# Optimization experiments

Hardware: AMD Instinct MI355X
Metric: run time of the kernel (lower is better)

The kernel has to match this reference:

```python
import jax, jax.numpy as jnp
import numpy as np

DIN = 256
HID = 512

def setup_inputs() -> dict:
    key = jax.random.key(0)
    ks = jax.random.split(key, 9)
    s_in = 1.0 / np.sqrt(DIN)
    s_h = 1.0 / np.sqrt(HID)
    h = jax.random.normal(ks[0], (32, 1024, DIN), dtype=jnp.float32)
    Wv = jax.random.uniform(ks[1], (HID, DIN), jnp.float32, -s_in, s_in)
    bv = jax.random.uniform(ks[2], (HID,), jnp.float32, -s_in, s_in)
    Wk = jax.random.uniform(ks[3], (HID, DIN), jnp.float32, -s_in, s_in)
    bk = jax.random.uniform(ks[4], (HID,), jnp.float32, -s_in, s_in)
    Wq = jax.random.uniform(ks[5], (HID, DIN), jnp.float32, -s_in, s_in)
    bq = jax.random.uniform(ks[6], (HID,), jnp.float32, -s_in, s_in)
    Wo = jax.random.uniform(ks[7], (DIN, HID), jnp.float32, -s_h, s_h)
    bo = jax.random.uniform(ks[8], (DIN,), jnp.float32, -s_h, s_h)
    return {"h": h, "Wv": Wv, "bv": bv, "Wk": Wk, "bk": bk, "Wq": Wq, "bq": bq, "Wo": Wo, "bo": bo}

def reference(h, Wv, bv, Wk, bk, Wq, bq, Wo, bo):
    # relu-activated Q/K/V projections: [B, N, HID]
    v = jax.nn.relu(jnp.einsum('bnd,hd->bnh', h, Wv) + bv)
    q = jax.nn.relu(jnp.einsum('bnd,hd->bnh', h, Wq) + bq)
    k = jax.nn.relu(jnp.einsum('bnd,hd->bnh', h, Wk) + bk)
    # unscaled attention: [B, N, N]
    att = jax.nn.softmax(jnp.einsum('bnh,bmh->bnm', q, k), axis=2)
    out = jnp.einsum('bnm,bmh->bnh', att, v)          # [B, N, HID]
    out = jax.nn.relu(jnp.einsum('bnh,dh->bnd', out, Wo) + bo)  # [B, N, DIN]
    return out
```

## Files before the change

### kernel.cpp

```cpp
#include <hip/hip_runtime.h>
#include <cstdint>
#include <cstddef>

#define NB    32
#define SEQ   1024
#define DIN   256
#define HID   512
#define MTOT  32768
#define KQLD  1024

typedef _Float16 half_t;
typedef _Float16 half8  __attribute__((ext_vector_type(8)));
typedef _Float16 half4v __attribute__((ext_vector_type(4)));
typedef float    f32x4  __attribute__((ext_vector_type(4)));

typedef __attribute__((address_space(1))) const void* gas_ptr;
typedef __attribute__((address_space(3))) void*       las_ptr;

__global__ void cvt_all(const float* __restrict__ h,
                        const float* __restrict__ Wv, const float* __restrict__ Wk,
                        const float* __restrict__ Wq, const float* __restrict__ Wo,
                        const float* __restrict__ bv, const float* __restrict__ bk,
                        const float* __restrict__ bq,
                        half_t* __restrict__ h16, half_t* __restrict__ W16,
                        half_t* __restrict__ Wo16, float* __restrict__ biasq) {
    int b = blockIdx.x;
    if (b < 8192) {
        int i = b * 256 + threadIdx.x;
        f32x4 v = ((const f32x4*)h)[i];
        half4v o;
        o[0] = (half_t)v[0]; o[1] = (half_t)v[1]; o[2] = (half_t)v[2]; o[3] = (half_t)v[3];
        ((half4v*)h16)[i] = o;
    } else if (b < 8704) {
        int w = (b - 8192) >> 7;
        int i = ((b - 8192) & 127) * 256 + threadIdx.x;
        const float* s = w == 0 ? Wv : w == 1 ? Wk : w == 2 ? Wq : Wo;
        half_t*      d = w < 3 ? W16 + (size_t)w * HID * DIN : Wo16;
        f32x4 v = ((const f32x4*)s)[i];
        half4v o;
        o[0] = (half_t)v[0]; o[1] = (half_t)v[1]; o[2] = (half_t)v[2]; o[3] = (half_t)v[3];
        ((half4v*)d)[i] = o;
    } else {
        for (int i = threadIdx.x; i < HID; i += 256) {
            biasq[i]           = bv[i];
            biasq[HID + i]     = bk[i];
            biasq[2 * HID + i] = bq[i];
        }
    }
}

__global__ __launch_bounds__(256, 2) void kq_k(
    const half_t* __restrict__ A, const half_t* __restrict__ Bw,
    const float* __restrict__ biasq, half_t* __restrict__ kq16)
{
    __shared__ alignas(16) half_t As[128 * 32];
    __shared__ alignas(16) half_t Bs[256 * 32];

    const int t    = threadIdx.x;
    const int lane = t & 63;
    const int wave = t >> 6;
    const int wm   = wave >> 1;
    const int wn   = wave & 1;
    const int lanen = lane & 15;
    const int quad  = lane >> 4;
    const long m0 = (long)blockIdx.x * 128;
    const long n0 = (long)blockIdx.y * 256;

    const half_t* gA[2]; half_t* lA[2];
    const half_t* gB[4]; half_t* lB[4];
#pragma unroll
    for (int s = 0; s < 2; s++) {
        int c = t + 256 * s;
        gA[s] = A + (m0 + (c >> 2)) * DIN + (c & 3) * 8;
        lA[s] = &As[c * 8];
    }
#pragma unroll
    for (int s = 0; s < 4; s++) {
        int c = t + 256 * s;
        gB[s] = Bw + (n0 + (c >> 2)) * DIN + (c & 3) * 8;
        lB[s] = &Bs[c * 8];
    }

    int aoff[4], boff[8];
#pragma unroll
    for (int i = 0; i < 4; i++) aoff[i] = (wm * 64 + i * 16 + lanen) * 32 + quad * 8;
#pragma unroll
    for (int j = 0; j < 8; j++) boff[j] = (wn * 128 + j * 16 + lanen) * 32 + quad * 8;

    f32x4 acc[4][8];
#pragma unroll
    for (int i = 0; i < 4; i++)
#pragma unroll
        for (int j = 0; j < 8; j++)
            acc[i][j] = f32x4{0.f, 0.f, 0.f, 0.f};

    for (int k0 = 0; k0 < DIN; k0 += 32) {
#pragma unroll
        for (int s = 0; s < 2; s++)
            __builtin_amdgcn_global_load_lds((gas_ptr)(gA[s] + k0), (las_ptr)lA[s], 16, 0, 0);
#pragma unroll
        for (int s = 0; s < 4; s++)
            __builtin_amdgcn_global_load_lds((gas_ptr)(gB[s] + k0), (las_ptr)lB[s], 16, 0, 0);
        __syncthreads();
        half8 af[4], bf[8];
#pragma unroll
        for (int i = 0; i < 4; i++) af[i] = *(const half8*)&As[aoff[i]];
#pragma unroll
        for (int j = 0; j < 8; j++) bf[j] = *(const half8*)&Bs[boff[j]];
#pragma unroll
        for (int i = 0; i < 4; i++)
#pragma unroll
            for (int j = 0; j < 8; j++)
                acc[i][j] = __builtin_amdgcn_mfma_f32_16x16x32_f16(bf[j], af[i], acc[i][j], 0, 0, 0);
        __syncthreads();
    }

#pragma unroll
    for (int i = 0; i < 4; i++) {
        long mrow = m0 + wm * 64 + i * 16 + lanen;
#pragma unroll
        for (int j = 0; j < 8; j++) {
            long gn = n0 + wn * 128 + j * 16 + quad * 4;
            f32x4 bb = *(const f32x4*)&biasq[HID + gn];
            f32x4 v = acc[i][j];
            half4v pk;
#pragma unroll
            for (int r = 0; r < 4; r++) pk[r] = (half_t)fmaxf(v[r] + bb[r], 0.f);
            *(half4v*)(kq16 + mrow * KQLD + gn) = pk;
        }
    }
}

__global__ __launch_bounds__(256, 2) void v_k(
    const half_t* __restrict__ A, const half_t* __restrict__ Bw,
    const float* __restrict__ biasq, half_t* __restrict__ vT)
{
    __shared__ alignas(16) half_t As[128 * 32];
    __shared__ alignas(16) half_t Bs[256 * 32];

    const int t    = threadIdx.x;
    const int lane = t & 63;
    const int wave = t >> 6;
    const int wm   = wave >> 1;
    const int wn   = wave & 1;
    const int lanen = lane & 15;
    const int quad  = lane >> 4;
    const long m0 = (long)blockIdx.x * 128;
    const long n0 = (long)blockIdx.y * 256;

    const half_t* gA[2]; half_t* lA[2];
    const half_t* gB[4]; half_t* lB[4];
#pragma unroll
    for (int s = 0; s < 2; s++) {
        int c = t + 256 * s;
        gA[s] = A + (m0 + (c >> 2)) * DIN + (c & 3) * 8;
        lA[s] = &As[c * 8];
    }
#pragma unroll
    for (int s = 0; s < 4; s++) {
        int c = t + 256 * s;
        gB[s] = Bw + (n0 + (c >> 2)) * DIN + (c & 3) * 8;
        lB[s] = &Bs[c * 8];
    }

    int aoff[4], boff[8];
#pragma unroll
    for (int i = 0; i < 4; i++) aoff[i] = (wm * 64 + i * 16 + lanen) * 32 + quad * 8;
#pragma unroll
    for (int j = 0; j < 8; j++) boff[j] = (wn * 128 + j * 16 + lanen) * 32 + quad * 8;

    f32x4 acc[4][8];
#pragma unroll
    for (int i = 0; i < 4; i++)
#pragma unroll
        for (int j = 0; j < 8; j++)
            acc[i][j] = f32x4{0.f, 0.f, 0.f, 0.f};

    for (int k0 = 0; k0 < DIN; k0 += 32) {
#pragma unroll
        for (int s = 0; s < 2; s++)
            __builtin_amdgcn_global_load_lds((gas_ptr)(gA[s] + k0), (las_ptr)lA[s], 16, 0, 0);
#pragma unroll
        for (int s = 0; s < 4; s++)
            __builtin_amdgcn_global_load_lds((gas_ptr)(gB[s] + k0), (las_ptr)lB[s], 16, 0, 0);
        __syncthreads();
        half8 af[4], bf[8];
#pragma unroll
        for (int i = 0; i < 4; i++) af[i] = *(const half8*)&As[aoff[i]];
#pragma unroll
        for (int j = 0; j < 8; j++) bf[j] = *(const half8*)&Bs[boff[j]];
#pragma unroll
        for (int i = 0; i < 4; i++)
#pragma unroll
            for (int j = 0; j < 8; j++)
                acc[i][j] = __builtin_amdgcn_mfma_f32_16x16x32_f16(af[i], bf[j], acc[i][j], 0, 0, 0);
        __syncthreads();
    }

#pragma unroll
    for (int i = 0; i < 4; i++) {
        long mrow = m0 + wm * 64 + i * 16 + quad * 4;
        long bidx = mrow >> 10;
        long pos  = mrow & 1023;
#pragma unroll
        for (int j = 0; j < 8; j++) {
            long gn = n0 + wn * 128 + j * 16 + lanen;
            float bb = biasq[gn];
            f32x4 v = acc[i][j];
            half4v pk;
#pragma unroll
            for (int r = 0; r < 4; r++) pk[r] = (half_t)fmaxf(v[r] + bb, 0.f);
            *(half4v*)(vT + ((bidx * HID + gn) << 10) + pos) = pk;
        }
    }
}

__global__ __launch_bounds__(256, 2) void se_k(
    const half_t* __restrict__ KQ,
    half_t* __restrict__ E, float* __restrict__ Mstat, float* __restrict__ Lstat)
{
    __shared__ alignas(16) half_t As[128 * 32];
    __shared__ alignas(16) half_t Bs[256 * 32];

    const int t    = threadIdx.x;
    const int lane = t & 63;
    const int wave = t >> 6;
    const int wm   = wave >> 1;
    const int wn   = wave & 1;
    const int lanen = lane & 15;
    const int quad  = lane >> 4;
    const int z     = blockIdx.z;
    const long m0 = (long)blockIdx.x * 128;
    const long n0 = (long)blockIdx.y * 256;

    const half_t* Ab = KQ + (long)z * SEQ * KQLD + HID;
    const half_t* Bb = KQ + (long)z * SEQ * KQLD;

    f32x4 acc[4][8];
#pragma unroll
    for (int i = 0; i < 4; i++)
#pragma unroll
        for (int j = 0; j < 8; j++)
            acc[i][j] = f32x4{0.f, 0.f, 0.f, 0.f};

    const half_t* gA[2]; half_t* lA[2];
    const half_t* gB[4]; half_t* lB[4];
#pragma unroll
    for (int s = 0; s < 2; s++) {
        int c = t + 256 * s;
        gA[s] = Ab + (m0 + (c >> 2)) * KQLD + (c & 3) * 8;
        lA[s] = &As[c * 8];
    }
#pragma unroll
    for (int s = 0; s < 4; s++) {
        int c = t + 256 * s;
        gB[s] = Bb + (n0 + (c >> 2)) * KQLD + (c & 3) * 8;
        lB[s] = &Bs[c * 8];
    }

    int aoff[4], boff[8];
#pragma unroll
    for (int i = 0; i < 4; i++) aoff[i] = (wm * 64 + i * 16 + lanen) * 32 + quad * 8;
#pragma unroll
    for (int j = 0; j < 8; j++) boff[j] = (wn * 128 + j * 16 + lanen) * 32 + quad * 8;

    for (int k0 = 0; k0 < HID; k0 += 32) {
#pragma unroll
        for (int s = 0; s < 2; s++)
            __builtin_amdgcn_global_load_lds((gas_ptr)(gA[s] + k0), (las_ptr)lA[s], 16, 0, 0);
#pragma unroll
        for (int s = 0; s < 4; s++)
            __builtin_amdgcn_global_load_lds((gas_ptr)(gB[s] + k0), (las_ptr)lB[s], 16, 0, 0);
        __syncthreads();

        half8 af[4], bf[8];
#pragma unroll
        for (int i = 0; i < 4; i++) af[i] = *(const half8*)&As[aoff[i]];
#pragma unroll
        for (int j = 0; j < 8; j++) bf[j] = *(const half8*)&Bs[boff[j]];
#pragma unroll
        for (int i = 0; i < 4; i++)
#pragma unroll
            for (int j = 0; j < 8; j++)
                acc[i][j] = __builtin_amdgcn_mfma_f32_16x16x32_f16(bf[j], af[i], acc[i][j], 0, 0, 0);
        __syncthreads();
    }

    float mf[4];
#pragma unroll
    for (int i = 0; i < 4; i++) {
        float v = acc[i][0][0];
#pragma unroll
        for (int j = 0; j < 8; j++)
#pragma unroll
            for (int r = 0; r < 4; r++) v = fmaxf(v, acc[i][j][r]);
        v = fmaxf(v, __shfl_xor(v, 16, 64));
        v = fmaxf(v, __shfl_xor(v, 32, 64));
        mf[i] = v;
    }

    half_t* Eb = E + (long)z * SEQ * SEQ;
    float rs[4] = {0.f, 0.f, 0.f, 0.f};
#pragma unroll
    for (int i = 0; i < 4; i++) {
        long qrow = m0 + wm * 64 + i * 16 + lanen;
#pragma unroll
        for (int j = 0; j < 8; j++) {
            long gn = n0 + wn * 128 + j * 16 + quad * 4;
            half4v hv;
#pragma unroll
            for (int r = 0; r < 4; r++) {
                float e = __expf(acc[i][j][r] - mf[i]);
                rs[i] += e;
                hv[r] = (half_t)e;
            }
            *(half4v*)(Eb + qrow * SEQ + gn) = hv;
        }
    }
#pragma unroll
    for (int i = 0; i < 4; i++) {
        float v = rs[i];
        v += __shfl_xor(v, 16, 64);
        v += __shfl_xor(v, 32, 64);
        rs[i] = v;
    }

    if (quad == 0) {
        long base = ((long)z * 8 + blockIdx.y * 2 + wn) * SEQ + m0 + wm * 64;
#pragma unroll
        for (int i = 0; i < 4; i++) {
            Mstat[base + i * 16 + lanen] = mf[i];
            Lstat[base + i * 16 + lanen] = rs[i];
        }
    }
}

__global__ __launch_bounds__(256, 2) void pv_k(
    const half_t* __restrict__ E, const half_t* __restrict__ vT,
    const float* __restrict__ Mstat, const float* __restrict__ Lstat,
    half_t* __restrict__ O16)
{
    __shared__ alignas(16) half_t As[128 * 32];
    __shared__ alignas(16) half_t Bs[256 * 32];
    __shared__ float scaleS[8][128];
    __shared__ float invS[128];

    const int t    = threadIdx.x;
    const int lane = t & 63;
    const int wave = t >> 6;
    const int wm   = wave >> 1;
    const int wn   = wave & 1;
    const int lanen = lane & 15;
    const int quad  = lane >> 4;
    const int z     = blockIdx.z;
    const long m0 = (long)blockIdx.x * 128;
    const long h0 = (long)blockIdx.y * 256;

    if (t < 128) {
        float mv[8];
        float M = -1e30f;
#pragma unroll
        for (int kb = 0; kb < 8; kb++) {
            mv[kb] = Mstat[((long)z * 8 + kb) * SEQ + m0 + t];
            M = fmaxf(M, mv[kb]);
        }
        float ls = 0.f;
#pragma unroll
        for (int kb = 0; kb < 8; kb++) {
            float sc = __expf(mv[kb] - M);
            scaleS[kb][t] = sc;
            ls += Lstat[((long)z * 8 + kb) * SEQ + m0 + t] * sc;
        }
        invS[t] = 1.f / ls;
    }
    __syncthreads();

    const half_t* Ab = E  + (long)z * SEQ * SEQ;
    const half_t* Bb = vT + (long)z * HID * SEQ;

    f32x4 acc[4][8];
#pragma unroll
    for (int i = 0; i < 4; i++)
#pragma unroll
        for (int j = 0; j < 8; j++)
            acc[i][j] = f32x4{0.f, 0.f, 0.f, 0.f};

    const half_t* gA[2]; half_t* lA[2];
    const half_t* gB[4]; half_t* lB[4];
#pragma unroll
    for (int s = 0; s < 2; s++) {
        int c = t + 256 * s;
        gA[s] = Ab + (m0 + (c >> 2)) * SEQ + (c & 3) * 8;
        lA[s] = &As[c * 8];
    }
#pragma unroll
    for (int s = 0; s < 4; s++) {
        int c = t + 256 * s;
        gB[s] = Bb + (h0 + (c >> 2)) * SEQ + (c & 3) * 8;
        lB[s] = &Bs[c * 8];
    }

    int aoff[4], boff[8];
#pragma unroll
    for (int i = 0; i < 4; i++) aoff[i] = (wm * 64 + i * 16 + lanen) * 32 + quad * 8;
#pragma unroll
    for (int j = 0; j < 8; j++) boff[j] = (wn * 128 + j * 16 + lanen) * 32 + quad * 8;

    for (int k0 = 0; k0 < SEQ; k0 += 32) {
#pragma unroll
        for (int s = 0; s < 2; s++)
            __builtin_amdgcn_global_load_lds((gas_ptr)(gA[s] + k0), (las_ptr)lA[s], 16, 0, 0);
#pragma unroll
        for (int s = 0; s < 4; s++)
            __builtin_amdgcn_global_load_lds((gas_ptr)(gB[s] + k0), (las_ptr)lB[s], 16, 0, 0);
        __syncthreads();

        const int kb = k0 >> 7;
        half8 af[4], bf[8];
#pragma unroll
        for (int i = 0; i < 4; i++) {
            af[i] = *(const half8*)&As[aoff[i]];
            half_t sh = (half_t)scaleS[kb][wm * 64 + i * 16 + lanen];
            af[i] *= sh;
        }
#pragma unroll
        for (int j = 0; j < 8; j++) bf[j] = *(const half8*)&Bs[boff[j]];
#pragma unroll
        for (int i = 0; i < 4; i++)
#pragma unroll
            for (int j = 0; j < 8; j++)
                acc[i][j] = __builtin_amdgcn_mfma_f32_16x16x32_f16(bf[j], af[i], acc[i][j], 0, 0, 0);
        __syncthreads();
    }

    half_t* o = O16 + (long)z * SEQ * KQLD;
#pragma unroll
    for (int i = 0; i < 4; i++) {
        int qrl = wm * 64 + i * 16 + lanen;
        long qrow = m0 + qrl;
        float inv = invS[qrl];
#pragma unroll
        for (int j = 0; j < 8; j++) {
            long gn = h0 + wn * 128 + j * 16 + quad * 4;
            half4v hv;
#pragma unroll
            for (int r = 0; r < 4; r++) hv[r] = (half_t)(acc[i][j][r] * inv);
            *(half4v*)(o + qrow * KQLD + gn) = hv;
        }
    }
}

__global__ __launch_bounds__(256, 2) void oproj_k(
    const half_t* __restrict__ A, const half_t* __restrict__ Bw,
    float* __restrict__ Out, const float* __restrict__ bias)
{
    __shared__ alignas(16) half_t As[128 * 32];
    __shared__ alignas(16) half_t Bs[128 * 32];

    const int t    = threadIdx.x;
    const int lane = t & 63;
    const int wave = t >> 6;
    const int wm   = wave >> 1;
    const int wn   = wave & 1;
    const int lanen = lane & 15;
    const int quad  = lane >> 4;
    const long m0 = (long)blockIdx.x * 128;
    const long n0 = (long)blockIdx.y * 128;

    f32x4 acc[4][4];
#pragma unroll
    for (int i = 0; i < 4; i++)
#pragma unroll
        for (int j = 0; j < 4; j++)
            acc[i][j] = f32x4{0.f, 0.f, 0.f, 0.f};

    const int c0 = t, c1 = t + 256;
    const half_t* gA0 = A  + (m0 + (c0 >> 2)) * KQLD + (c0 & 3) * 8;
    const half_t* gA1 = A  + (m0 + (c1 >> 2)) * KQLD + (c1 & 3) * 8;
    const half_t* gB0 = Bw + (n0 + (c0 >> 2)) * HID + (c0 & 3) * 8;
    const half_t* gB1 = Bw + (n0 + (c1 >> 2)) * HID + (c1 & 3) * 8;
    half_t* lA0 = &As[c0 * 8];
    half_t* lA1 = &As[c1 * 8];
    half_t* lB0 = &Bs[c0 * 8];
    half_t* lB1 = &Bs[c1 * 8];

    int aoff[4], boff[4];
#pragma unroll
    for (int i = 0; i < 4; i++) aoff[i] = (wm * 64 + i * 16 + lanen) * 32 + quad * 8;
#pragma unroll
    for (int j = 0; j < 4; j++) boff[j] = (wn * 64 + j * 16 + lanen) * 32 + quad * 8;

    for (int k0 = 0; k0 < HID; k0 += 32) {
        __builtin_amdgcn_global_load_lds((gas_ptr)(gA0 + k0), (las_ptr)lA0, 16, 0, 0);
        __builtin_amdgcn_global_load_lds((gas_ptr)(gA1 + k0), (las_ptr)lA1, 16, 0, 0);
        __builtin_amdgcn_global_load_lds((gas_ptr)(gB0 + k0), (las_ptr)lB0, 16, 0, 0);
        __builtin_amdgcn_global_load_lds((gas_ptr)(gB1 + k0), (las_ptr)lB1, 16, 0, 0);
        __syncthreads();

        half8 af[4], bf[4];
#pragma unroll
        for (int i = 0; i < 4; i++) af[i] = *(const half8*)&As[aoff[i]];
#pragma unroll
        for (int j = 0; j < 4; j++) bf[j] = *(const half8*)&Bs[boff[j]];
#pragma unroll
        for (int i = 0; i < 4; i++)
#pragma unroll
            for (int j = 0; j < 4; j++)
                acc[i][j] = __builtin_amdgcn_mfma_f32_16x16x32_f16(bf[j], af[i], acc[i][j], 0, 0, 0);
        __syncthreads();
    }

#pragma unroll
    for (int i = 0; i < 4; i++) {
        long mrow = m0 + wm * 64 + i * 16 + lanen;
#pragma unroll
        for (int j = 0; j < 4; j++) {
            long gn = n0 + wn * 64 + j * 16 + quad * 4;
            f32x4 bb = *(const f32x4*)&bias[gn];
            f32x4 v = acc[i][j];
            f32x4 ov;
#pragma unroll
            for (int r = 0; r < 4; r++) ov[r] = fmaxf(v[r] + bb[r], 0.f);
            *(f32x4*)&Out[mrow * DIN + gn] = ov;
        }
    }
}

extern "C" void kernel_launch(void* const* d_in, const int* in_sizes, int n_in,
                              void* d_out, int out_size, void* d_ws, size_t ws_size,
                              hipStream_t stream) {
    const float* h  = (const float*)d_in[0];
    const float* Wv = (const float*)d_in[1];
    const float* bv = (const float*)d_in[2];
    const float* Wk = (const float*)d_in[3];
    const float* bk = (const float*)d_in[4];
    const float* Wq = (const float*)d_in[5];
    const float* bq = (const float*)d_in[6];
    const float* Wo = (const float*)d_in[7];
    const float* bo = (const float*)d_in[8];

    uint8_t* ws = (uint8_t*)d_ws;
    size_t off = 0;
    auto alloc = [&](size_t bytes) { size_t o = off; off += (bytes + 255) & ~(size_t)255; return o; };

    half_t* W16   = (half_t*)(ws + alloc((size_t)3 * HID * DIN * 2));
    half_t* Wo16  = (half_t*)(ws + alloc((size_t)DIN * HID * 2));
    float*  biasq = (float*)(ws + alloc((size_t)3 * HID * 4));
    half_t* kq16  = (half_t*)(ws + alloc((size_t)MTOT * KQLD * 2));
    half_t* vT    = (half_t*)(ws + alloc((size_t)MTOT * HID * 2));
    size_t h16_off = alloc((size_t)MTOT * DIN * 2);
    half_t* h16   = (half_t*)(ws + h16_off);
    half_t* O16 = kq16;

    size_t s_avail = ws_size > h16_off ? ws_size - h16_off : 0;
    size_t per_batch = (size_t)SEQ * SEQ * 2 + 2 * 8 * SEQ * 4;
    int GB = (int)(s_avail / per_batch);
    if (GB > NB) GB = NB;
    if (GB < 1)  GB = 1;
    half_t* Ebuf  = (half_t*)(ws + h16_off);
    float*  Mstat = (float*)(ws + h16_off + (size_t)GB * SEQ * SEQ * 2);
    float*  Lstat = Mstat + (size_t)GB * 8 * SEQ;

    cvt_all<<<dim3(8705), 256, 0, stream>>>(h, Wv, Wk, Wq, Wo, bv, bk, bq,
                                            h16, W16, Wo16, biasq);

    kq_k<<<dim3(MTOT / 128, 4), 256, 0, stream>>>(h16, W16 + (size_t)HID * DIN, biasq, kq16);
    v_k<<<dim3(MTOT / 128, 2), 256, 0, stream>>>(h16, W16, biasq, vT);

    for (int g0 = 0; g0 < NB; g0 += GB) {
        int gb = NB - g0 < GB ? NB - g0 : GB;
        se_k<<<dim3(SEQ / 128, SEQ / 256, gb), 256, 0, stream>>>(
            kq16 + (size_t)g0 * SEQ * KQLD,
            Ebuf, Mstat, Lstat);
        pv_k<<<dim3(SEQ / 128, HID / 256, gb), 256, 0, stream>>>(
            Ebuf, vT + (size_t)g0 * HID * SEQ,
            Mstat, Lstat,
            O16 + (size_t)g0 * SEQ * KQLD);
    }

    oproj_k<<<dim3(MTOT / 128, DIN / 128), 256, 0, stream>>>(O16, Wo16, (float*)d_out, bo);

    (void)in_sizes; (void)n_in; (void)out_size;
}
```

Before: 310.3 us.

## Double-buffer LDS tiles to overlap global-to-LDS loads with MFMA in all GEMMs

Every GEMM kernel (K/Q projection, V projection, score/exp, PV, output projection) now uses two LDS buffers for its A and B tiles. The first tile is loaded before the loop, and each iteration prefetches the next k-slice into the other buffer right after the barrier. The trailing per-iteration barrier is removed, and so is the separate barrier after the scale setup in the PV kernel. The aim is to hide global_load_lds latency behind MFMA work and halve the number of barriers. In exchange, LDS use per block doubles, which could limit occupancy.

Measured after the change: 315.1 us. Within noise of the previous version (+1.6%).

```diff
diff --git a/kernel.cpp b/kernel.cpp
--- a/kernel.cpp
+++ b/kernel.cpp
@@ -53,8 +53,8 @@
     const half_t* __restrict__ A, const half_t* __restrict__ Bw,
     const float* __restrict__ biasq, half_t* __restrict__ kq16)
 {
-    __shared__ alignas(16) half_t As[128 * 32];
-    __shared__ alignas(16) half_t Bs[256 * 32];
+    __shared__ alignas(16) half_t As[2][128 * 32];
+    __shared__ alignas(16) half_t Bs[2][256 * 32];
 
     const int t    = threadIdx.x;
     const int lane = t & 63;
@@ -66,19 +66,19 @@
     const long m0 = (long)blockIdx.x * 128;
     const long n0 = (long)blockIdx.y * 256;
 
-    const half_t* gA[2]; half_t* lA[2];
-    const half_t* gB[4]; half_t* lB[4];
+    const half_t* gA[2]; const half_t* gB[4];
+    int lAo[2], lBo[4];
 #pragma unroll
     for (int s = 0; s < 2; s++) {
         int c = t + 256 * s;
         gA[s] = A + (m0 + (c >> 2)) * DIN + (c & 3) * 8;
-        lA[s] = &As[c * 8];
+        lAo[s] = c * 8;
     }
 #pragma unroll
     for (int s = 0; s < 4; s++) {
         int c = t + 256 * s;
         gB[s] = Bw + (n0 + (c >> 2)) * DIN + (c & 3) * 8;
-        lB[s] = &Bs[c * 8];
+        lBo[s] = c * 8;
     }
 
     int aoff[4], boff[8];
@@ -94,25 +94,36 @@
         for (int j = 0; j < 8; j++)
             acc[i][j] = f32x4{0.f, 0.f, 0.f, 0.f};
 
-    for (int k0 = 0; k0 < DIN; k0 += 32) {
-#pragma unroll
-        for (int s = 0; s < 2; s++)
-            __builtin_amdgcn_global_load_lds((gas_ptr)(gA[s] + k0), (las_ptr)lA[s], 16, 0, 0);
-#pragma unroll
-        for (int s = 0; s < 4; s++)
-            __builtin_amdgcn_global_load_lds((gas_ptr)(gB[s] + k0), (las_ptr)lB[s], 16, 0, 0);
+#pragma unroll
+    for (int s = 0; s < 2; s++)
+        __builtin_amdgcn_global_load_lds((gas_ptr)gA[s], (las_ptr)&As[0][lAo[s]], 16, 0, 0);
+#pragma unroll
+    for (int s = 0; s < 4; s++)
+        __builtin_amdgcn_global_load_lds((gas_ptr)gB[s], (las_ptr)&Bs[0][lBo[s]], 16, 0, 0);
+
+#pragma unroll 2
+    for (int it = 0; it < DIN / 32; ++it) {
+        const int cur = it & 1;
         __syncthreads();
+        if (it + 1 < DIN / 32) {
+            const int k1 = (it + 1) * 32;
+#pragma unroll
+            for (int s = 0; s < 2; s++)
+                __builtin_amdgcn_global_load_lds((gas_ptr)(gA[s] + k1), (las_ptr)&As[cur ^ 1][lAo[s]], 16, 0, 0);
+#pragma unroll
+            for (int s = 0; s < 4; s++)
+                __builtin_amdgcn_global_load_lds((gas_ptr)(gB[s] + k1), (las_ptr)&Bs[cur ^ 1][lBo[s]], 16, 0, 0);
+        }
         half8 af[4], bf[8];
 #pragma unroll
-        for (int i = 0; i < 4; i++) af[i] = *(const half8*)&As[aoff[i]];
-#pragma unroll
-        for (int j = 0; j < 8; j++) bf[j] = *(const half8*)&Bs[boff[j]];
+        for (int i = 0; i < 4; i++) af[i] = *(const half8*)&As[cur][aoff[i]];
+#pragma unroll
+        for (int j = 0; j < 8; j++) bf[j] = *(const half8*)&Bs[cur][boff[j]];
 #pragma unroll
         for (int i = 0; i < 4; i++)
 #pragma unroll
             for (int j = 0; j < 8; j++)
                 acc[i][j] = __builtin_amdgcn_mfma_f32_16x16x32_f16(bf[j], af[i], acc[i][j], 0, 0, 0);
-        __syncthreads();
     }
 
 #pragma unroll
@@ -135,8 +146,8 @@
     const half_t* __restrict__ A, const half_t* __restrict__ Bw,
     const float* __restrict__ biasq, half_t* __restrict__ vT)
 {
-    __shared__ alignas(16) half_t As[128 * 32];
-    __shared__ alignas(16) half_t Bs[256 * 32];
+    __shared__ alignas(16) half_t As[2][128 * 32];
+    __shared__ alignas(16) half_t Bs[2][256 * 32];
 
     const int t    = threadIdx.x;
     const int lane = t & 63;
@@ -148,19 +159,19 @@
     const long m0 = (long)blockIdx.x * 128;
     const long n0 = (long)blockIdx.y * 256;
 
-    const half_t* gA[2]; half_t* lA[2];
-    const half_t* gB[4]; half_t* lB[4];
+    const half_t* gA[2]; const half_t* gB[4];
+    int lAo[2], lBo[4];
 #pragma unroll
     for (int s = 0; s < 2; s++) {
         int c = t + 256 * s;
         gA[s] = A + (m0 + (c >> 2)) * DIN + (c & 3) * 8;
-        lA[s] = &As[c * 8];
+        lAo[s] = c * 8;
     }
 #pragma unroll
     for (int s = 0; s < 4; s++) {
         int c = t + 256 * s;
         gB[s] = Bw + (n0 + (c >> 2)) * DIN + (c & 3) * 8;
-        lB[s] = &Bs[c * 8];
+        lBo[s] = c * 8;
     }
 
     int aoff[4], boff[8];
@@ -176,25 +187,36 @@
         for (int j = 0; j < 8; j++)
             acc[i][j] = f32x4{0.f, 0.f, 0.f, 0.f};
 
-    for (int k0 = 0; k0 < DIN; k0 += 32) {
-#pragma unroll
-        for (int s = 0; s < 2; s++)
-            __builtin_amdgcn_global_load_lds((gas_ptr)(gA[s] + k0), (las_ptr)lA[s], 16, 0, 0);
-#pragma unroll
-        for (int s = 0; s < 4; s++)
-            __builtin_amdgcn_global_load_lds((gas_ptr)(gB[s] + k0), (las_ptr)lB[s], 16, 0, 0);
+#pragma unroll
+    for (int s = 0; s < 2; s++)
+        __builtin_amdgcn_global_load_lds((gas_ptr)gA[s], (las_ptr)&As[0][lAo[s]], 16, 0, 0);
+#pragma unroll
+    for (int s = 0; s < 4; s++)
+        __builtin_amdgcn_global_load_lds((gas_ptr)gB[s], (las_ptr)&Bs[0][lBo[s]], 16, 0, 0);
+
+#pragma unroll 2
+    for (int it = 0; it < DIN / 32; ++it) {
+        const int cur = it & 1;
         __syncthreads();
+        if (it + 1 < DIN / 32) {
+            const int k1 = (it + 1) * 32;
+#pragma unroll
+            for (int s = 0; s < 2; s++)
+                __builtin_amdgcn_global_load_lds((gas_ptr)(gA[s] + k1), (las_ptr)&As[cur ^ 1][lAo[s]], 16, 0, 0);
+#pragma unroll
+            for (int s = 0; s < 4; s++)
+                __builtin_amdgcn_global_load_lds((gas_ptr)(gB[s] + k1), (las_ptr)&Bs[cur ^ 1][lBo[s]], 16, 0, 0);
+        }
         half8 af[4], bf[8];
 #pragma unroll
-        for (int i = 0; i < 4; i++) af[i] = *(const half8*)&As[aoff[i]];
-#pragma unroll
-        for (int j = 0; j < 8; j++) bf[j] = *(const half8*)&Bs[boff[j]];
+        for (int i = 0; i < 4; i++) af[i] = *(const half8*)&As[cur][aoff[i]];
+#pragma unroll
+        for (int j = 0; j < 8; j++) bf[j] = *(const half8*)&Bs[cur][boff[j]];
 #pragma unroll
         for (int i = 0; i < 4; i++)
 #pragma unroll
             for (int j = 0; j < 8; j++)
                 acc[i][j] = __builtin_amdgcn_mfma_f32_16x16x32_f16(af[i], bf[j], acc[i][j], 0, 0, 0);
-        __syncthreads();
     }
 
 #pragma unroll
@@ -219,8 +241,8 @@
     const half_t* __restrict__ KQ,
     half_t* __restrict__ E, float* __restrict__ Mstat, float* __restrict__ Lstat)
 {
-    __shared__ alignas(16) half_t As[128 * 32];
-    __shared__ alignas(16) half_t Bs[256 * 32];
+    __shared__ alignas(16) half_t As[2][128 * 32];
+    __shared__ alignas(16) half_t Bs[2][256 * 32];
 
     const int t    = threadIdx.x;
     const int lane = t & 63;
@@ -243,19 +265,19 @@
         for (int j = 0; j < 8; j++)
             acc[i][j] = f32x4{0.f, 0.f, 0.f, 0.f};
 
-    const half_t* gA[2]; half_t* lA[2];
-    const half_t* gB[4]; half_t* lB[4];
+    const half_t* gA[2]; const half_t* gB[4];
+    int lAo[2], lBo[4];
 #pragma unroll
     for (int s = 0; s < 2; s++) {
         int c = t + 256 * s;
         gA[s] = Ab + (m0 + (c >> 2)) * KQLD + (c & 3) * 8;
-        lA[s] = &As[c * 8];
+        lAo[s] = c * 8;
     }
 #pragma unroll
     for (int s = 0; s < 4; s++) {
         int c = t + 256 * s;
         gB[s] = Bb + (n0 + (c >> 2)) * KQLD + (c & 3) * 8;
-        lB[s] = &Bs[c * 8];
+        lBo[s] = c * 8;
     }
 
     int aoff[4], boff[8];
@@ -264,26 +286,36 @@
 #pragma unroll
     for (int j = 0; j < 8; j++) boff[j] = (wn * 128 + j * 16 + lanen) * 32 + quad * 8;
 
-    for (int k0 = 0; k0 < HID; k0 += 32) {
-#pragma unroll
-        for (int s = 0; s < 2; s++)
-            __builtin_amdgcn_global_load_lds((gas_ptr)(gA[s] + k0), (las_ptr)lA[s], 16, 0, 0);
-#pragma unroll
-        for (int s = 0; s < 4; s++)
-            __builtin_amdgcn_global_load_lds((gas_ptr)(gB[s] + k0), (las_ptr)lB[s], 16, 0, 0);
+#pragma unroll
+    for (int s = 0; s < 2; s++)
+        __builtin_amdgcn_global_load_lds((gas_ptr)gA[s], (las_ptr)&As[0][lAo[s]], 16, 0, 0);
+#pragma unroll
+    for (int s = 0; s < 4; s++)
+        __builtin_amdgcn_global_load_lds((gas_ptr)gB[s], (las_ptr)&Bs[0][lBo[s]], 16, 0, 0);
+
+#pragma unroll 2
+    for (int it = 0; it < HID / 32; ++it) {
+        const int cur = it & 1;
         __syncthreads();
-
+        if (it + 1 < HID / 32) {
+            const int k1 = (it + 1) * 32;
+#pragma unroll
+            for (int s = 0; s < 2; s++)
+                __builtin_amdgcn_global_load_lds((gas_ptr)(gA[s] + k1), (las_ptr)&As[cur ^ 1][lAo[s]], 16, 0, 0);
+#pragma unroll
+            for (int s = 0; s < 4; s++)
+                __builtin_amdgcn_global_load_lds((gas_ptr)(gB[s] + k1), (las_ptr)&Bs[cur ^ 1][lBo[s]], 16, 0, 0);
+        }
         half8 af[4], bf[8];
 #pragma unroll
-        for (int i = 0; i < 4; i++) af[i] = *(const half8*)&As[aoff[i]];
-#pragma unroll
-        for (int j = 0; j < 8; j++) bf[j] = *(const half8*)&Bs[boff[j]];
+        for (int i = 0; i < 4; i++) af[i] = *(const half8*)&As[cur][aoff[i]];
+#pragma unroll
+        for (int j = 0; j < 8; j++) bf[j] = *(const half8*)&Bs[cur][boff[j]];
 #pragma unroll
         for (int i = 0; i < 4; i++)
 #pragma unroll
             for (int j = 0; j < 8; j++)
                 acc[i][j] = __builtin_amdgcn_mfma_f32_16x16x32_f16(bf[j], af[i], acc[i][j], 0, 0, 0);
-        __syncthreads();
     }
 
     float mf[4];
@@ -340,8 +372,8 @@
     const float* __restrict__ Mstat, const float* __restrict__ Lstat,
     half_t* __restrict__ O16)
 {
-    __shared__ alignas(16) half_t As[128 * 32];
-    __shared__ alignas(16) half_t Bs[256 * 32];
+    __shared__ alignas(16) half_t As[2][128 * 32];
+    __shared__ alignas(16) half_t Bs[2][256 * 32];
     __shared__ float scaleS[8][128];
     __shared__ float invS[128];
 
@@ -373,7 +405,6 @@
         }
         invS[t] = 1.f / ls;
     }
-    __syncthreads();
 
     const half_t* Ab = E  + (long)z * SEQ * SEQ;
     const half_t* Bb = vT + (long)z * HID * SEQ;
@@ -385,19 +416,19 @@
         for (int j = 0; j < 8; j++)
             acc[i][j] = f32x4{0.f, 0.f, 0.f, 0.f};
 
-    const half_t* gA[2]; half_t* lA[2];
-    const half_t* gB[4]; half_t* lB[4];
+    const half_t* gA[2]; const half_t* gB[4];
+    int lAo[2], lBo[4];
 #pragma unroll
     for (int s = 0; s < 2; s++) {
         int c = t + 256 * s;
         gA[s] = Ab + (m0 + (c >> 2)) * SEQ + (c & 3) * 8;
-        lA[s] = &As[c * 8];
+        lAo[s] = c * 8;
     }
 #pragma unroll
     for (int s = 0; s < 4; s++) {
         int c = t + 256 * s;
         gB[s] = Bb + (h0 + (c >> 2)) * SEQ + (c & 3) * 8;
-        lB[s] = &Bs[c * 8];
+        lBo[s] = c * 8;
     }
 
     int aoff[4], boff[8];
@@ -406,31 +437,41 @@
 #pragma unroll
     for (int j = 0; j < 8; j++) boff[j] = (wn * 128 + j * 16 + lanen) * 32 + quad * 8;
 
-    for (int k0 = 0; k0 < SEQ; k0 += 32) {
-#pragma unroll
-        for (int s = 0; s < 2; s++)
-            __builtin_amdgcn_global_load_lds((gas_ptr)(gA[s] + k0), (las_ptr)lA[s], 16, 0, 0);
-#pragma unroll
-        for (int s = 0; s < 4; s++)
-            __builtin_amdgcn_global_load_lds((gas_ptr)(gB[s] + k0), (las_ptr)lB[s], 16, 0, 0);
+#pragma unroll
+    for (int s = 0; s < 2; s++)
+        __builtin_amdgcn_global_load_lds((gas_ptr)gA[s], (las_ptr)&As[0][lAo[s]], 16, 0, 0);
+#pragma unroll
+    for (int s = 0; s < 4; s++)
+        __builtin_amdgcn_global_load_lds((gas_ptr)gB[s], (las_ptr)&Bs[0][lBo[s]], 16, 0, 0);
+
+#pragma unroll 2
+    for (int it = 0; it < SEQ / 32; ++it) {
+        const int cur = it & 1;
         __syncthreads();
-
-        const int kb = k0 >> 7;
+        if (it + 1 < SEQ / 32) {
+            const int k1 = (it + 1) * 32;
+#pragma unroll
+            for (int s = 0; s < 2; s++)
+                __builtin_amdgcn_global_load_lds((gas_ptr)(gA[s] + k1), (las_ptr)&As[cur ^ 1][lAo[s]], 16, 0, 0);
+#pragma unroll
+            for (int s = 0; s < 4; s++)
+                __builtin_amdgcn_global_load_lds((gas_ptr)(gB[s] + k1), (las_ptr)&Bs[cur ^ 1][lBo[s]], 16, 0, 0);
+        }
+        const int kb = it >> 2;
         half8 af[4], bf[8];
 #pragma unroll
         for (int i = 0; i < 4; i++) {
-            af[i] = *(const half8*)&As[aoff[i]];
+            af[i] = *(const half8*)&As[cur][aoff[i]];
             half_t sh = (half_t)scaleS[kb][wm * 64 + i * 16 + lanen];
             af[i] *= sh;
         }
 #pragma unroll
-        for (int j = 0; j < 8; j++) bf[j] = *(const half8*)&Bs[boff[j]];
+        for (int j = 0; j < 8; j++) bf[j] = *(const half8*)&Bs[cur][boff[j]];
 #pragma unroll
         for (int i = 0; i < 4; i++)
 #pragma unroll
             for (int j = 0; j < 8; j++)
                 acc[i][j] = __builtin_amdgcn_mfma_f32_16x16x32_f16(bf[j], af[i], acc[i][j], 0, 0, 0);
-        __syncthreads();
     }
 
     half_t* o = O16 + (long)z * SEQ * KQLD;
@@ -454,8 +495,8 @@
     const half_t* __restrict__ A, const half_t* __restrict__ Bw,
     float* __restrict__ Out, const float* __restrict__ bias)
 {
-    __shared__ alignas(16) half_t As[128 * 32];
-    __shared__ alignas(16) half_t Bs[128 * 32];
+    __shared__ alignas(16) half_t As[2][128 * 32];
+    __shared__ alignas(16) half_t Bs[2][128 * 32];
 
     const int t    = threadIdx.x;
     const int lane = t & 63;
@@ -479,10 +520,7 @@
     const half_t* gA1 = A  + (m0 + (c1 >> 2)) * KQLD + (c1 & 3) * 8;
     const half_t* gB0 = Bw + (n0 + (c0 >> 2)) * HID + (c0 & 3) * 8;
     const half_t* gB1 = Bw + (n0 + (c1 >> 2)) * HID + (c1 & 3) * 8;
-    half_t* lA0 = &As[c0 * 8];
-    half_t* lA1 = &As[c1 * 8];
-    half_t* lB0 = &Bs[c0 * 8];
-    half_t* lB1 = &Bs[c1 * 8];
+    const int lA0 = c0 * 8, lA1 = c1 * 8, lB0 = c0 * 8, lB1 = c1 * 8;
 
     int aoff[4], boff[4];
 #pragma unroll
@@ -490,24 +528,32 @@
 #pragma unroll
     for (int j = 0; j < 4; j++) boff[j] = (wn * 64 + j * 16 + lanen) * 32 + quad * 8;
 
-    for (int k0 = 0; k0 < HID; k0 += 32) {
-        __builtin_amdgcn_global_load_lds((gas_ptr)(gA0 + k0), (las_ptr)lA0, 16, 0, 0);
-        __builtin_amdgcn_global_load_lds((gas_ptr)(gA1 + k0), (las_ptr)lA1, 16, 0, 0);
-        __builtin_amdgcn_global_load_lds((gas_ptr)(gB0 + k0), (las_ptr)lB0, 16, 0, 0);
-        __builtin_amdgcn_global_load_lds((gas_ptr)(gB1 + k0), (las_ptr)lB1, 16, 0, 0);
+    __builtin_amdgcn_global_load_lds((gas_ptr)gA0, (las_ptr)&As[0][lA0], 16, 0, 0);
+    __builtin_amdgcn_global_load_lds((gas_ptr)gA1, (las_ptr)&As[0][lA1], 16, 0, 0);
+    __builtin_amdgcn_global_load_lds((gas_ptr)gB0, (las_ptr)&Bs[0][lB0], 16, 0, 0);
+    __builtin_amdgcn_global_load_lds((gas_ptr)gB1, (las_ptr)&Bs[0][lB1], 16, 0, 0);
+
+#pragma unroll 2
+    for (int it = 0; it < HID / 32; ++it) {
+        const int cur = it & 1;
         __syncthreads();
-
+        if (it + 1 < HID / 32) {
+            const int k1 = (it + 1) * 32;
+            __builtin_amdgcn_global_load_lds((gas_ptr)(gA0 + k1), (las_ptr)&As[cur ^ 1][lA0], 16, 0, 0);
+            __builtin_amdgcn_global_load_lds((gas_ptr)(gA1 + k1), (las_ptr)&As[cur ^ 1][lA1], 16, 0, 0);
+            __builtin_amdgcn_global_load_lds((gas_ptr)(gB0 + k1), (las_ptr)&Bs[cur ^ 1][lB0], 16, 0, 0);
+            __builtin_amdgcn_global_load_lds((gas_ptr)(gB1 + k1), (las_ptr)&Bs[cur ^ 1][lB1], 16, 0, 0);
+        }
         half8 af[4], bf[4];
 #pragma unroll
-        for (int i = 0; i < 4; i++) af[i] = *(const half8*)&As[aoff[i]];
-#pragma unroll
-        for (int j = 0; j < 4; j++) bf[j] = *(const half8*)&Bs[boff[j]];
+        for (int i = 0; i < 4; i++) af[i] = *(const half8*)&As[cur][aoff[i]];
+#pragma unroll
+        for (int j = 0; j < 4; j++) bf[j] = *(const half8*)&Bs[cur][boff[j]];
 #pragma unroll
         for (int i = 0; i < 4; i++)
 #pragma unroll
             for (int j = 0; j < 4; j++)
                 acc[i][j] = __builtin_amdgcn_mfma_f32_16x16x32_f16(bf[j], af[i], acc[i][j], 0, 0, 0);
-        __syncthreads();
     }
 
 #pragma unroll
```
